# Kernel tuning notes

Hardware: AMD Instinct MI355X
Metric: run time of the kernel (lower is better)

The kernel has to match this reference:

```python
import jax, jax.numpy as jnp
import numpy as np

N = 20000   # nodes
E = 320000  # edges
T = 12      # sequence_length
H = 64      # hidden_dim
CIN = 16    # input_dim_per_step
L = 3       # num_st_layers
BN_EPS = 1e-5


def setup_inputs() -> dict:
    key = jax.random.key(0)
    ks = jax.random.split(key, 30)
    s = 0.05
    rn = lambda k, shp: jax.random.normal(k, shp, jnp.float32) * s
    inp = {
        "x": jax.random.normal(ks[0], (N, T * CIN), jnp.float32),
        "edge_index": jax.random.randint(ks[1], (2, E), 0, N, jnp.int32),
        # embedding
        "We": rn(ks[2], (CIN, H)), "be": rn(ks[3], (H,)),
        # stacked per-layer params for the 3 ST layers
        "gcn_W": rn(ks[4], (L, H, H)), "gcn_b": rn(ks[5], (L, H)),
        "conv_w": rn(ks[6], (L, H, H, 3)), "conv_b": rn(ks[7], (L, H)),
        "bn_g": jnp.ones((L, H), jnp.float32), "bn_b": rn(ks[8], (L, H)),
        "bn_m": rn(ks[9], (L, H)),
        "bn_v": jax.random.uniform(ks[10], (L, H), jnp.float32, 0.5, 1.5),
        # temporal attention MLP (H -> H//2 -> 1)
        "ta_w1": rn(ks[11], (H, H // 2)), "ta_b1": rn(ks[12], (H // 2,)),
        "ta_w2": rn(ks[13], (H // 2, 1)), "ta_b2": rn(ks[14], (1,)),
        # feature attention MLP (T -> T//2 -> 1)
        "fa_w1": rn(ks[15], (T, T // 2)), "fa_b1": rn(ks[16], (T // 2,)),
        "fa_w2": rn(ks[17], (T // 2, 1)), "fa_b2": rn(ks[18], (1,)),
        # output MLP (H -> H//2 -> 1)
        "ow1": rn(ks[19], (H, H // 2)), "ob1": rn(ks[20], (H // 2,)),
        "ow2": rn(ks[21], (H // 2, 1)), "ob2": rn(ks[22], (1,)),
    }
    return inp


def reference(x, edge_index, We, be, gcn_W, gcn_b, conv_w, conv_b,
              bn_g, bn_b, bn_m, bn_v, ta_w1, ta_b1, ta_w2, ta_b2,
              fa_w1, fa_b1, fa_w2, fa_b2, ow1, ob1, ow2, ob2):
    n = x.shape[0]
    # --- GCN normalization with self-loops (PyG gcn_norm) ---
    loops = jnp.arange(n, dtype=edge_index.dtype)
    src = jnp.concatenate([edge_index[0], loops])
    dst = jnp.concatenate([edge_index[1], loops])
    deg = jax.ops.segment_sum(jnp.ones_like(src, jnp.float32), dst, num_segments=n)
    dinv = 1.0 / jnp.sqrt(deg)  # deg >= 1 thanks to self-loops
    coef = dinv[src] * dinv[dst]  # [E+N]

    # --- per-timestep embedding (vectorized over t) ---
    xr = x.reshape(n, T, CIN)
    emb = jax.nn.relu(jnp.einsum('ntc,ch->nth', xr, We) + be)  # [N,T,H]
    x_st = emb.reshape(n, T * H)

    # --- ST layers (replicating original row-major .view layout mixing) ---
    for i in range(L):
        xi = x_st.reshape(n, H, T)  # [N,C,T]
        # GCNConv per timestep, batched over t: linear then normalized aggregate
        h = jnp.einsum('nct,cd->ndt', xi, gcn_W[i])          # [N,H,T]
        msg = coef[:, None, None] * h[src]                   # [E+N,H,T]
        agg = jax.ops.segment_sum(msg, dst, num_segments=n) + gcn_b[i][None, :, None]
        # temporal conv (kernel 3, pad 1) over T
        tmp = jax.lax.conv_general_dilated(
            agg, conv_w[i], (1,), [(1, 1)],
            dimension_numbers=('NCH', 'OIH', 'NCH')) + conv_b[i][None, :, None]
        # BatchNorm1d (eval mode: running stats)
        normed = (tmp - bn_m[i][None, :, None]) / jnp.sqrt(bn_v[i][None, :, None] + BN_EPS)
        normed = normed * bn_g[i][None, :, None] + bn_b[i][None, :, None]
        # residual is Identity (in_channels == out_channels)
        x_st = jax.nn.relu(normed + xi).reshape(n, H * T)

    # --- dual attention pooling ---
    xa = x_st.reshape(n, T, H)
    tw = (jnp.einsum('ntm,mk->ntk', jax.nn.relu(jnp.einsum('nth,hm->ntm', xa, ta_w1) + ta_b1), ta_w2) + ta_b2)[..., 0]
    tw = jax.nn.softmax(tw, axis=1)                          # [N,T]
    xt = (xa * tw[..., None]).transpose(0, 2, 1)             # [N,H,T]
    fw = (jnp.einsum('nhm,mk->nhk', jax.nn.relu(jnp.einsum('nht,tm->nhm', xt, fa_w1) + fa_b1), fa_w2) + fa_b2)[..., 0]
    fw = jax.nn.softmax(fw, axis=1)                          # [N,H]
    x_final = jnp.sum(xt * fw[..., None], axis=2)            # [N,H]

    # --- output MLP (dropout is identity in eval) ---
    out = jax.nn.relu(x_final @ ow1 + ob1) @ ow2 + ob2       # [N,1]
    return out
```

## Files before the change

kernel.cpp:

```cpp
#include <hip/hip_runtime.h>
#include <cstddef>
#include <cstdint>

#define T_ 12
#define H_ 64
#define CIN_ 16
#define F_ 768
#define PAD_ROW 772
#define BN_EPS 1e-5f
#define ECAP 80
#define RPITCH 88

typedef float v2f __attribute__((ext_vector_type(2)));
typedef short s8v __attribute__((ext_vector_type(8)));
typedef float f4v __attribute__((ext_vector_type(4)));

__device__ __forceinline__ unsigned short f2bf(float f) {
    unsigned u = __float_as_uint(f);
    unsigned r = (u + 0x7FFFu + ((u >> 16) & 1u)) >> 16;
    return (unsigned short)r;
}
__device__ __forceinline__ float bf2f(unsigned short h) {
    return __uint_as_float(((unsigned)h) << 16);
}
__device__ __forceinline__ v2f bf2x2(unsigned u) {
    v2f r;
    r.x = __uint_as_float(u << 16);
    r.y = __uint_as_float(u & 0xFFFF0000u);
    return r;
}
__device__ __forceinline__ v2f pkfma(v2f a, v2f b, v2f c) {
    return __builtin_elementwise_fma(a, b, c);
}


__global__ void k_init(int* __restrict__ cnt, int* __restrict__ cursor, int n) {
    int i = blockIdx.x * 256 + threadIdx.x;
    if (i < n) { cnt[i] = 0; cursor[i] = 0; }
}

__global__ void k_count(const int* __restrict__ dstv, int* __restrict__ cnt, int e) {
    int i = blockIdx.x * 256 + threadIdx.x;
    if (i < e) atomicAdd(&cnt[dstv[i]], 1);
}

__global__ __launch_bounds__(1024) void k_scan1(const int* __restrict__ cnt,
                                                int* __restrict__ row_local,
                                                int* __restrict__ bsum, int n) {
    __shared__ int sd[1024];
    int tid = threadIdx.x;
    int i = blockIdx.x * 1024 + tid;
    int v = (i < n) ? cnt[i] : 0;
    sd[tid] = v;
    __syncthreads();
    for (int off = 1; off < 1024; off <<= 1) {
        int t = (tid >= off) ? sd[tid - off] : 0;
        __syncthreads();
        sd[tid] += t;
        __syncthreads();
    }
    if (i < n) row_local[i] = sd[tid] - v;
    if (tid == 1023) bsum[blockIdx.x] = sd[1023];
}

__global__ __launch_bounds__(64) void k_scan2(const int* __restrict__ bsum,
                                              int* __restrict__ boff, int nb,
                                              int* __restrict__ row_start, int n) {
    int lane = threadIdx.x;
    int orig = (lane < nb) ? bsum[lane] : 0;
    int v = orig;
    for (int off = 1; off < 64; off <<= 1) {
        int t = __shfl_up(v, off);
        if (lane >= off) v += t;
    }
    if (lane < nb) boff[lane] = v - orig;
    if (lane == 63) row_start[n] = v;
}

__global__ __launch_bounds__(1024) void k_scan3(const int* __restrict__ row_local,
                                                const int* __restrict__ boff,
                                                const int* __restrict__ cnt,
                                                int* __restrict__ row_start,
                                                float* __restrict__ dinv, int n) {
    int i = blockIdx.x * 1024 + threadIdx.x;
    if (i < n) {
        row_start[i] = row_local[i] + boff[blockIdx.x];
        dinv[i] = rsqrtf((float)(cnt[i] + 1));
    }
}

__global__ void k_scatter(const int* __restrict__ srcv, const int* __restrict__ dstv,
                          const int* __restrict__ row_start, int* __restrict__ cursor,
                          const float* __restrict__ dinv, int* __restrict__ csr_src,
                          float* __restrict__ csr_coef, int e) {
    int i = blockIdx.x * 256 + threadIdx.x;
    if (i < e) {
        int d = dstv[i], s = srcv[i];
        int pos = atomicAdd(&cursor[d], 1);
        int idx = row_start[d] + pos;
        csr_src[idx]  = s;
        csr_coef[idx] = dinv[s] * dinv[d];
    }
}


__global__ __launch_bounds__(256) void k_wprep(const float* __restrict__ gcn_W,
                                               const float* __restrict__ gcn_b,
                                               const float* __restrict__ conv_w,
                                               float* __restrict__ wkp,
                                               float* __restrict__ bkp) {
    int b = blockIdx.x;
    int l = b / 12, k = (b / 4) % 3, cq = b & 3;
    const float* Wg = gcn_W + (size_t)l * 4096;
    const float* cw = conv_w + (size_t)l * 12288;
    int tid = threadIdx.x;
#pragma unroll
    for (int j = 0; j < 4; j++) {
        int idx = j * 256 + tid;
        int c = cq * 16 + (idx >> 6);
        int o = idx & 63;
        float acc = 0.f;
        for (int d = 0; d < 64; d++)
            acc += Wg[c * 64 + d] * cw[(size_t)(o * 64 + d) * 3 + k];
        wkp[(((size_t)l * 3 + k) * 64 + c) * 64 + o] = acc;
    }
    if (cq == 0 && tid < 64) {
        int o = tid;
        const float* gb = gcn_b + (size_t)l * 64;
        float acc = 0.f;
        for (int d = 0; d < 64; d++)
            acc += gb[d] * cw[(size_t)(o * 64 + d) * 3 + k];
        bkp[((size_t)l * 3 + k) * 64 + o] = acc;
    }
}

__global__ __launch_bounds__(64) void k_wpack(const float* __restrict__ wkp,
                                              unsigned short* __restrict__ wkA) {
    int b = blockIdx.x;
    int l = b / 24, rem = b % 24;
    int mt = rem / 6, ks = rem % 6;
    int lane = threadIdx.x;
    int o = mt * 16 + (lane & 15);
    int kbase = ks * 32 + (lane >> 4) * 8;
#pragma unroll
    for (int j = 0; j < 8; j++) {
        int k = kbase + j;
        int kk = k >> 6, c = k & 63;
        float v = wkp[(((size_t)l * 3 + kk) * 64 + c) * 64 + o];
        wkA[((((size_t)l * 24) + mt * 6 + ks) * 64 + lane) * 8 + j] = f2bf(v);
    }
}


__global__ __launch_bounds__(256) void k_embed(const float* __restrict__ x,
                                               const float* __restrict__ We,
                                               const float* __restrict__ be,
                                               unsigned short* __restrict__ xbf,
                                               int nT) {
    __shared__ float sW[CIN_ * H_];
    __shared__ float sb[H_];
    for (int i = threadIdx.x; i < CIN_ * H_; i += 256) sW[i] = We[i];
    if (threadIdx.x < H_) sb[threadIdx.x] = be[threadIdx.x];
    __syncthreads();
    int h4  = threadIdx.x & 15;
    int ntl = threadIdx.x >> 4;
    int nt  = blockIdx.x * 16 + ntl;
    if (nt >= nT) return;
    const float4* xp = (const float4*)(x + (size_t)nt * CIN_);
    float4 xv4[4];
    xv4[0] = xp[0]; xv4[1] = xp[1]; xv4[2] = xp[2]; xv4[3] = xp[3];
    const float* xs = (const float*)xv4;
    float acc[4];
#pragma unroll
    for (int j = 0; j < 4; j++) acc[j] = sb[h4 * 4 + j];
#pragma unroll
    for (int c = 0; c < CIN_; c++) {
        float4 w = *(const float4*)&sW[c * H_ + h4 * 4];
        float xc = xs[c];
        acc[0] += xc * w.x; acc[1] += xc * w.y; acc[2] += xc * w.z; acc[3] += xc * w.w;
    }
    ushort4 h;
    h.x = f2bf(fmaxf(acc[0], 0.f)); h.y = f2bf(fmaxf(acc[1], 0.f));
    h.z = f2bf(fmaxf(acc[2], 0.f)); h.w = f2bf(fmaxf(acc[3], 0.f));
    *(ushort4*)&xbf[(size_t)nt * H_ + h4 * 4] = h;
}


#define BPK(aL, aH, c2, u) { \
    aL = pkfma(bf2x2((u).x), c2, aL); \
    aH = pkfma(bf2x2((u).y), c2, aH); }

__global__ __launch_bounds__(256, 6) void k_layer(
        const unsigned short* __restrict__ xin,
        unsigned short* __restrict__ xout,
        const int* __restrict__ row_start, const int* __restrict__ csr_src,
        const float* __restrict__ csr_coef, const float* __restrict__ dinv,
        const unsigned short* __restrict__ wkA,
        const float* __restrict__ bkp,
        const float* __restrict__ cb,
        const float* __restrict__ bng, const float* __restrict__ bnb,
        const float* __restrict__ bnm, const float* __restrict__ bnv,
        int n) {
    __shared__ unsigned short sxb[8 * 14 * RPITCH];
    __shared__ int se[4 * ECAP * 2];
    int tid = threadIdx.x;
    int n0 = blockIdx.x * 8;
    int wave = tid >> 6, lane = tid & 63;
    int wbase = wave * (ECAP * 2);

    for (int i = tid; i < 8 * 2 * RPITCH; i += 256) {
        int s = i / (2 * RPITCH);
        int r = i - s * (2 * RPITCH);
        int row = (r < RPITCH) ? 0 : 13;
        int c = (r < RPITCH) ? r : r - RPITCH;
        sxb[s * 14 * RPITCH + row * RPITCH + c] = 0;
    }

    int begs[2], cnts[2], stgs[2], epos[2];
    {
        int pos = 0;
#pragma unroll
        for (int si = 0; si < 2; si++) {
            int nn = n0 + wave * 2 + si; if (nn >= n) nn = n - 1;
            int beg = row_start[nn], end = row_start[nn + 1];
            int cnt = end - beg;
            int stg = min(cnt, ECAP - pos);
            for (int i = lane; i < stg; i += 64) {
                se[wbase + (pos + i) * 2]     = csr_src[beg + i];
                se[wbase + (pos + i) * 2 + 1] = __float_as_int(csr_coef[beg + i]);
            }
            begs[si] = beg; cnts[si] = cnt; stgs[si] = stg; epos[si] = pos;
            pos += stg;
        }
    }

    {
        int i0 = 3 * lane;
#pragma unroll
        for (int si = 0; si < 2; si++) {
            int s = wave * 2 + si;
            int nn = n0 + s; if (nn >= n) nn = n - 1;
            float dn = dinv[nn];
            float cs = dn * dn;
            v2f cs2 = {cs, cs};
            const uint2* xp = (const uint2*)(xin + (size_t)nn * F_);
            uint2 u0 = xp[i0], u1 = xp[i0 + 1], u2 = xp[i0 + 2];
            v2f a0 = bf2x2(u0.x) * cs2, a1 = bf2x2(u0.y) * cs2;
            v2f a2 = bf2x2(u1.x) * cs2, a3 = bf2x2(u1.y) * cs2;
            v2f a4 = bf2x2(u2.x) * cs2, a5 = bf2x2(u2.y) * cs2;
            int cnt = stgs[si];
            int base = wbase + epos[si] * 2;
            int e = 0;
            for (; e + 3 < cnt; e += 4) {
                int2 p0 = *(const int2*)&se[base + e * 2];
                int2 p1 = *(const int2*)&se[base + e * 2 + 2];
                int2 p2 = *(const int2*)&se[base + e * 2 + 4];
                int2 p3 = *(const int2*)&se[base + e * 2 + 6];
                const uint2* pA = (const uint2*)(xin + (size_t)p0.x * F_);
                const uint2* pB = (const uint2*)(xin + (size_t)p1.x * F_);
                const uint2* pC = (const uint2*)(xin + (size_t)p2.x * F_);
                const uint2* pD = (const uint2*)(xin + (size_t)p3.x * F_);
                uint2 uA0 = pA[i0], uA1 = pA[i0 + 1], uA2 = pA[i0 + 2];
                uint2 uB0 = pB[i0], uB1 = pB[i0 + 1], uB2 = pB[i0 + 2];
                uint2 uC0 = pC[i0], uC1 = pC[i0 + 1], uC2 = pC[i0 + 2];
                uint2 uD0 = pD[i0], uD1 = pD[i0 + 1], uD2 = pD[i0 + 2];
                float cA = __int_as_float(p0.y), cB = __int_as_float(p1.y);
                float cC = __int_as_float(p2.y), cD = __int_as_float(p3.y);
                v2f cA2 = {cA, cA}, cB2 = {cB, cB}, cC2 = {cC, cC}, cD2 = {cD, cD};
                BPK(a0, a1, cA2, uA0) BPK(a2, a3, cA2, uA1) BPK(a4, a5, cA2, uA2)
                BPK(a0, a1, cB2, uB0) BPK(a2, a3, cB2, uB1) BPK(a4, a5, cB2, uB2)
                BPK(a0, a1, cC2, uC0) BPK(a2, a3, cC2, uC1) BPK(a4, a5, cC2, uC2)
                BPK(a0, a1, cD2, uD0) BPK(a2, a3, cD2, uD1) BPK(a4, a5, cD2, uD2)
            }
            for (; e < cnt; e++) {
                int2 p0 = *(const int2*)&se[base + e * 2];
                const uint2* pA = (const uint2*)(xin + (size_t)p0.x * F_);
                uint2 uA0 = pA[i0], uA1 = pA[i0 + 1], uA2 = pA[i0 + 2];
                float cA = __int_as_float(p0.y);
                v2f cA2 = {cA, cA};
                BPK(a0, a1, cA2, uA0) BPK(a2, a3, cA2, uA1) BPK(a4, a5, cA2, uA2)
            }
            for (int g = begs[si] + stgs[si]; g < begs[si] + cnts[si]; g++) {
                int srcI = csr_src[g];
                float cf = csr_coef[g];
                const uint2* pA = (const uint2*)(xin + (size_t)srcI * F_);
                uint2 uA0 = pA[i0], uA1 = pA[i0 + 1], uA2 = pA[i0 + 2];
                v2f cf2 = {cf, cf};
                BPK(a0, a1, cf2, uA0) BPK(a2, a3, cf2, uA1) BPK(a4, a5, cf2, uA2)
            }
            unsigned short* wp = &sxb[s * 14 * RPITCH + RPITCH + lane];
            float vals[12] = {a0.x, a0.y, a1.x, a1.y, a2.x, a2.y,
                              a3.x, a3.y, a4.x, a4.y, a5.x, a5.y};
#pragma unroll
            for (int t = 0; t < 12; t++) wp[t * RPITCH] = f2bf(vals[t]);
        }
    }
    __syncthreads();

    {
        int mt = wave;
        int q = lane >> 4;
        int l15 = lane & 15;
        s8v afr[6];
        const s8v* Ap = (const s8v*)wkA;
#pragma unroll
        for (int ks = 0; ks < 6; ks++) afr[ks] = Ap[(mt * 6 + ks) * 64 + lane];
        int obase = mt * 16 + q * 4;
        float scl[4], shf[4], ball[4], bk0a[4], bk2a[4];
#pragma unroll
        for (int r = 0; r < 4; r++) {
            int o = obase + r;
            float sc = bng[o] * rsqrtf(bnv[o] + BN_EPS);
            scl[r] = sc;
            shf[r] = bnb[o] - bnm[o] * sc;
            float b0 = bkp[o], b1 = bkp[64 + o], b2 = bkp[128 + o];
            ball[r] = cb[o] + b0 + b1 + b2;
            bk0a[r] = b0; bk2a[r] = b2;
        }
#pragma unroll
        for (int nt = 0; nt < 6; nt++) {
            int nidx = nt * 16 + l15;
            int s = nidx / 12, t = nidx - 12 * s;
            const s8v* bp = (const s8v*)&sxb[s * 14 * RPITCH + t * RPITCH + q * 8];
            f4v acc = {0.f, 0.f, 0.f, 0.f};
            acc = __builtin_amdgcn_mfma_f32_16x16x32_bf16(afr[0], bp[0],  acc, 0, 0, 0);
            acc = __builtin_amdgcn_mfma_f32_16x16x32_bf16(afr[1], bp[4],  acc, 0, 0, 0);
            acc = __builtin_amdgcn_mfma_f32_16x16x32_bf16(afr[2], bp[11], acc, 0, 0, 0);
            acc = __builtin_amdgcn_mfma_f32_16x16x32_bf16(afr[3], bp[15], acc, 0, 0, 0);
            acc = __builtin_amdgcn_mfma_f32_16x16x32_bf16(afr[4], bp[22], acc, 0, 0, 0);
            acc = __builtin_amdgcn_mfma_f32_16x16x32_bf16(afr[5], bp[26], acc, 0, 0, 0);
            int nnode = n0 + s;
            bool valid = (nnode < n);
            int rn = valid ? nnode : (n - 1);
            const unsigned short* rrow = xin + (size_t)rn * F_;
            unsigned short* orow = xout + (size_t)rn * F_;
#pragma unroll
            for (int r = 0; r < 4; r++) {
                int o = obase + r;
                float bias = ball[r];
                if (t == 0)  bias -= bk0a[r];
                if (t == 11) bias -= bk2a[r];
                float v = (acc[r] + bias) * scl[r] + shf[r] + bf2f(rrow[o * 12 + t]);
                v = fmaxf(v, 0.f);
                if (valid) orow[o * 12 + t] = f2bf(v);
            }
        }
    }
}


__global__ __launch_bounds__(128) void k_attn(const unsigned short* __restrict__ xst,
        const float* __restrict__ taw1, const float* __restrict__ tab1,
        const float* __restrict__ taw2, const float* __restrict__ tab2,
        const float* __restrict__ faw1, const float* __restrict__ fab1,
        const float* __restrict__ faw2, const float* __restrict__ fab2,
        const float* __restrict__ ow1, const float* __restrict__ ob1,
        const float* __restrict__ ow2, const float* __restrict__ ob2,
        float* __restrict__ out, int n) {
    __shared__ float sT[8 * PAD_ROW];
    __shared__ float s_tab1[32], s_taw2[32], s_ob1[32], s_ow2[32];
    __shared__ float s_faw1[72], s_fab1[8], s_faw2[8];
    __shared__ float s_tw[8 * 12];
    __shared__ float s_xf[8 * 65];
    int tid = threadIdx.x;
    int n0 = blockIdx.x * 8;
    if (tid < 32) {
        s_tab1[tid] = tab1[tid]; s_taw2[tid] = taw2[tid];
        s_ob1[tid] = ob1[tid];   s_ow2[tid] = ow2[tid];
    }
    if (tid < 72) s_faw1[tid] = faw1[tid];
    if (tid < 6) { s_fab1[tid] = fab1[tid]; s_faw2[tid] = faw2[tid]; }
    float tb2 = tab2[0], fb2 = fab2[0], o_b2 = ob2[0];
    for (int i = tid; i < 8 * F_; i += 128) {
        int s = i / F_, j = i - s * F_;
        int t = j >> 6, hh = j & 63;
        int nn = n0 + s; if (nn >= n) nn = n - 1;
        sT[s * PAD_ROW + hh * 12 + t] = bf2f(xst[(size_t)nn * F_ + j]);
    }
    __syncthreads();

    int s = tid >> 4, m2 = tid & 15;
    {
        v2f a[12];
        v2f bb = *((const v2f*)s_tab1 + m2);
#pragma unroll
        for (int t = 0; t < 12; t++) a[t] = bb;
        const float* xr = &sT[s * PAD_ROW];
        const v2f* twp = (const v2f*)taw1 + m2;
        for (int hh = 0; hh < 64; hh++) {
            float4 q0 = *(const float4*)&xr[hh * 12];
            float4 q1 = *(const float4*)&xr[hh * 12 + 4];
            float4 q2 = *(const float4*)&xr[hh * 12 + 8];
            float xv[12] = {q0.x, q0.y, q0.z, q0.w, q1.x, q1.y, q1.z, q1.w, q2.x, q2.y, q2.z, q2.w};
            v2f wv = twp[hh * 16];
#pragma unroll
            for (int t = 0; t < 12; t++)
                a[t] = pkfma(wv, (v2f){xv[t], xv[t]}, a[t]);
        }
        float w20 = s_taw2[2 * m2], w21 = s_taw2[2 * m2 + 1];
#pragma unroll
        for (int t = 0; t < 12; t++) {
            float p = fmaxf(a[t].x, 0.f) * w20 + fmaxf(a[t].y, 0.f) * w21;
            p += __shfl_xor(p, 1); p += __shfl_xor(p, 2);
            p += __shfl_xor(p, 4); p += __shfl_xor(p, 8);
            if (m2 == 0) s_tw[s * 12 + t] = p + tb2;
        }
    }
    __syncthreads();

    int wave = tid >> 6, lane = tid & 63;
    for (int q = 0; q < 4; q++) {
        int ss = wave * 4 + q;
        float tw[12];
#pragma unroll
        for (int t = 0; t < 12; t++) tw[t] = s_tw[ss * 12 + t];
        float mx = tw[0];
#pragma unroll
        for (int t = 1; t < 12; t++) mx = fmaxf(mx, tw[t]);
        float sum = 0.f;
#pragma unroll
        for (int t = 0; t < 12; t++) { tw[t] = __expf(tw[t] - mx); sum += tw[t]; }
        float inv = 1.f / sum;
        const float* xr = &sT[ss * PAD_ROW + lane * 12];
        float4 q0 = *(const float4*)(xr);
        float4 q1 = *(const float4*)(xr + 4);
        float4 q2 = *(const float4*)(xr + 8);
        float xv[12] = {q0.x, q0.y, q0.z, q0.w, q1.x, q1.y, q1.z, q1.w, q2.x, q2.y, q2.z, q2.w};
        float xt[12];
#pragma unroll
        for (int t = 0; t < 12; t++) xt[t] = xv[t] * tw[t] * inv;
        float lf = fb2;
#pragma unroll
        for (int mm = 0; mm < 6; mm++) {
            float v = s_fab1[mm];
#pragma unroll
            for (int t = 0; t < 12; t++) v += xt[t] * s_faw1[t * 6 + mm];
            lf += fmaxf(v, 0.f) * s_faw2[mm];
        }
        float m2v = lf;
#pragma unroll
        for (int off = 32; off >= 1; off >>= 1) m2v = fmaxf(m2v, __shfl_xor(m2v, off));
        float e = __expf(lf - m2v);
        float se = e;
#pragma unroll
        for (int off = 32; off >= 1; off >>= 1) se += __shfl_xor(se, off);
        float fwv = e / se;
        float xs = 0.f;
#pragma unroll
        for (int t = 0; t < 12; t++) xs += xt[t];
        s_xf[ss * 65 + lane] = fwv * xs;
    }
    __syncthreads();

    {
        float v0 = s_ob1[2 * m2], v1 = s_ob1[2 * m2 + 1];
        const float* xfp = &s_xf[s * 65];
        for (int hh = 0; hh < 64; hh++) {
            float xv = xfp[hh];
            float2 wv = *(const float2*)&ow1[hh * 32 + 2 * m2];
            v0 += xv * wv.x;
            v1 += xv * wv.y;
        }
        float p = fmaxf(v0, 0.f) * s_ow2[2 * m2] + fmaxf(v1, 0.f) * s_ow2[2 * m2 + 1];
        p += __shfl_xor(p, 1); p += __shfl_xor(p, 2);
        p += __shfl_xor(p, 4); p += __shfl_xor(p, 8);
        if (m2 == 0 && n0 + s < n) out[n0 + s] = p + o_b2;
    }
}


extern "C" void kernel_launch(void* const* d_in, const int* in_sizes, int n_in,
                              void* d_out, int out_size, void* d_ws, size_t ws_size,
                              hipStream_t stream) {
    const float* x      = (const float*)d_in[0];
    const int*   ei     = (const int*)d_in[1];
    const float* We     = (const float*)d_in[2];
    const float* be     = (const float*)d_in[3];
    const float* gcn_W  = (const float*)d_in[4];
    const float* gcn_b  = (const float*)d_in[5];
    const float* conv_w = (const float*)d_in[6];
    const float* conv_b = (const float*)d_in[7];
    const float* bn_g   = (const float*)d_in[8];
    const float* bn_b   = (const float*)d_in[9];
    const float* bn_m   = (const float*)d_in[10];
    const float* bn_v   = (const float*)d_in[11];
    const float* ta_w1  = (const float*)d_in[12];
    const float* ta_b1  = (const float*)d_in[13];
    const float* ta_w2  = (const float*)d_in[14];
    const float* ta_b2  = (const float*)d_in[15];
    const float* fa_w1  = (const float*)d_in[16];
    const float* fa_b1  = (const float*)d_in[17];
    const float* fa_w2  = (const float*)d_in[18];
    const float* fa_b2  = (const float*)d_in[19];
    const float* ow1    = (const float*)d_in[20];
    const float* ob1    = (const float*)d_in[21];
    const float* ow2    = (const float*)d_in[22];
    const float* ob2    = (const float*)d_in[23];

    int n = in_sizes[0] / (T_ * CIN_);
    int e = in_sizes[1] / 2;
    const int* srcv = ei;
    const int* dstv = ei + e;

    char* p = (char*)d_ws;
    auto take = [&](size_t bytes) -> void* {
        void* r = (void*)p;
        p += (bytes + 255) & ~(size_t)255;
        return r;
    };
    int*   cnt       = (int*)take((size_t)n * 4);
    int*   cursor    = (int*)take((size_t)n * 4);
    int*   row_start = (int*)take(((size_t)n + 1) * 4);
    int*   row_local = (int*)take((size_t)n * 4);
    int*   bsum      = (int*)take(1024 * 4);
    int*   boff      = (int*)take(1024 * 4);
    float* dinv      = (float*)take((size_t)n * 4);
    int*   csr_src   = (int*)take((size_t)e * 4);
    float* csr_coef  = (float*)take((size_t)e * 4);
    float* wkp       = (float*)take((size_t)3 * 3 * 64 * 64 * 4);
    float* bkp       = (float*)take((size_t)3 * 3 * 64 * 4);
    unsigned short* wkA = (unsigned short*)take((size_t)3 * 24 * 64 * 8 * 2);
    unsigned short* xabf = (unsigned short*)take((size_t)n * F_ * 2);
    unsigned short* xbbf = (unsigned short*)take((size_t)n * F_ * 2);

    int nb_n = (n + 255) / 256;
    int nb_e = (e + 255) / 256;
    int nb_s = (n + 1023) / 1024;

    k_wprep<<<36, 256, 0, stream>>>(gcn_W, gcn_b, conv_w, wkp, bkp);
    k_wpack<<<72, 64, 0, stream>>>(wkp, wkA);
    k_init<<<nb_n, 256, 0, stream>>>(cnt, cursor, n);
    k_count<<<nb_e, 256, 0, stream>>>(dstv, cnt, e);
    k_scan1<<<nb_s, 1024, 0, stream>>>(cnt, row_local, bsum, n);
    k_scan2<<<1, 64, 0, stream>>>(bsum, boff, nb_s, row_start, n);
    k_scan3<<<nb_s, 1024, 0, stream>>>(row_local, boff, cnt, row_start, dinv, n);
    k_scatter<<<nb_e, 256, 0, stream>>>(srcv, dstv, row_start, cursor, dinv,
                                        csr_src, csr_coef, e);

    int nT = n * T_;
    k_embed<<<(nT + 15) / 16, 256, 0, stream>>>(x, We, be, xabf, nT);

    int nb8 = (n + 7) / 8;
    const unsigned short* curbf = xabf;
    for (int i = 0; i < 3; i++) {
        unsigned short* nxtbf = (curbf == xabf) ? xbbf : xabf;
        k_layer<<<nb8, 256, 0, stream>>>(curbf, nxtbf,
                                         row_start, csr_src, csr_coef, dinv,
                                         wkA + (size_t)i * 24 * 64 * 8,
                                         bkp + (size_t)i * 3 * 64,
                                         conv_b + (size_t)i * H_,
                                         bn_g + (size_t)i * H_, bn_b + (size_t)i * H_,
                                         bn_m + (size_t)i * H_, bn_v + (size_t)i * H_,
                                         n);
        curbf = nxtbf;
    }

    k_attn<<<nb8, 128, 0, stream>>>(curbf, ta_w1, ta_b1, ta_w2, ta_b2,
                                    fa_w1, fa_b1, fa_w2, fa_b2,
                                    ow1, ob1, ow2, ob2, (float*)d_out, n);
}
```

Measured before the change: 487.0 us.

## Degree-sort nodes for balanced layer blocks and vectorize residual epilogue

Adds a counting sort of nodes by in-degree and a permutation that puts heavy and light nodes together in each 8-node block (waves take ranks w and 7-w), so that per-block gather work in the layer kernel is more even. The layer epilogue now stages the BN output in shared memory and applies the residual add and ReLU with 16-byte coalesced loads and stores, replacing scattered 2-byte global accesses. The attention load also reads four bf16 values per access. In exchange there are four extra small setup kernels, and the permuted block order loses the locality that came from consecutive node ids.

```diff
diff --git a/kernel.cpp b/kernel.cpp
--- a/kernel.cpp
+++ b/kernel.cpp
@@ -10,6 +10,7 @@
 #define BN_EPS 1e-5f
 #define ECAP 80
 #define RPITCH 88
+#define DBINS 1024
 
 typedef float v2f __attribute__((ext_vector_type(2)));
 typedef short s8v __attribute__((ext_vector_type(8)));
@@ -34,9 +35,11 @@
 }
 
 
-__global__ void k_init(int* __restrict__ cnt, int* __restrict__ cursor, int n) {
+__global__ void k_init(int* __restrict__ cnt, int* __restrict__ cursor,
+                       int* __restrict__ hist, int* __restrict__ hcur, int n) {
     int i = blockIdx.x * 256 + threadIdx.x;
     if (i < n) { cnt[i] = 0; cursor[i] = 0; }
+    if (i < DBINS) { hist[i] = 0; hcur[i] = 0; }
 }
 
 __global__ void k_count(const int* __restrict__ dstv, int* __restrict__ cnt, int e) {
@@ -104,6 +107,53 @@
 }
 
 
+__global__ void k_hist(const int* __restrict__ cnt, int* __restrict__ hist, int n) {
+    int i = blockIdx.x * 256 + threadIdx.x;
+    if (i < n) {
+        int d = min(cnt[i], DBINS - 1);
+        atomicAdd(&hist[d], 1);
+    }
+}
+
+__global__ __launch_bounds__(1024) void k_hscan(const int* __restrict__ hist,
+                                                int* __restrict__ hoff, int n) {
+    __shared__ int sd[DBINS];
+    int tid = threadIdx.x;
+    int v = hist[tid];
+    sd[tid] = v;
+    __syncthreads();
+    for (int off = 1; off < DBINS; off <<= 1) {
+        int t = (tid >= off) ? sd[tid - off] : 0;
+        __syncthreads();
+        sd[tid] += t;
+        __syncthreads();
+    }
+    hoff[tid] = n - sd[tid];
+}
+
+__global__ void k_place(const int* __restrict__ cnt, const int* __restrict__ hoff,
+                        int* __restrict__ hcur, int* __restrict__ sorted, int n) {
+    int i = blockIdx.x * 256 + threadIdx.x;
+    if (i < n) {
+        int d = min(cnt[i], DBINS - 1);
+        int pos = atomicAdd(&hcur[d], 1);
+        sorted[hoff[d] + pos] = i;
+    }
+}
+
+__global__ void k_perm(const int* __restrict__ sorted, int* __restrict__ perm,
+                       int nb, int n) {
+    int i = blockIdx.x * 256 + threadIdx.x;
+    if (i < nb * 8) {
+        int b = i >> 3, s = i & 7;
+        int w = s >> 1, si = s & 1;
+        int j = si ? (7 - w) : w;
+        int rank = j * nb + b;
+        perm[i] = (rank < n) ? sorted[rank] : -1;
+    }
+}
+
+
 __global__ __launch_bounds__(256) void k_wprep(const float* __restrict__ gcn_W,
                                                const float* __restrict__ gcn_b,
                                                const float* __restrict__ conv_w,
@@ -195,13 +245,14 @@
         unsigned short* __restrict__ xout,
         const int* __restrict__ row_start, const int* __restrict__ csr_src,
         const float* __restrict__ csr_coef, const float* __restrict__ dinv,
+        const int* __restrict__ perm,
         const unsigned short* __restrict__ wkA,
         const float* __restrict__ bkp,
         const float* __restrict__ cb,
         const float* __restrict__ bng, const float* __restrict__ bnb,
         const float* __restrict__ bnm, const float* __restrict__ bnv,
         int n) {
-    __shared__ unsigned short sxb[8 * 14 * RPITCH];
+    __shared__ __align__(16) unsigned short sxb[8 * 14 * RPITCH];
     __shared__ int se[4 * ECAP * 2];
     int tid = threadIdx.x;
     int n0 = blockIdx.x * 8;
@@ -216,14 +267,16 @@
         sxb[s * 14 * RPITCH + row * RPITCH + c] = 0;
     }
 
-    int begs[2], cnts[2], stgs[2], epos[2];
+    int begs[2], cnts[2], stgs[2], epos[2], nodes[2];
     {
         int pos = 0;
 #pragma unroll
         for (int si = 0; si < 2; si++) {
-            int nn = n0 + wave * 2 + si; if (nn >= n) nn = n - 1;
+            int pmv = perm[n0 + wave * 2 + si];
+            int nn = (pmv >= 0) ? pmv : 0;
+            nodes[si] = pmv;
             int beg = row_start[nn], end = row_start[nn + 1];
-            int cnt = end - beg;
+            int cnt = (pmv >= 0) ? (end - beg) : 0;
             int stg = min(cnt, ECAP - pos);
             for (int i = lane; i < stg; i += 64) {
                 se[wbase + (pos + i) * 2]     = csr_src[beg + i];
@@ -239,7 +292,7 @@
 #pragma unroll
         for (int si = 0; si < 2; si++) {
             int s = wave * 2 + si;
-            int nn = n0 + s; if (nn >= n) nn = n - 1;
+            int nn = (nodes[si] >= 0) ? nodes[si] : 0;
             float dn = dinv[nn];
             float cs = dn * dn;
             v2f cs2 = {cs, cs};
@@ -297,54 +350,80 @@
     }
     __syncthreads();
 
-    {
-        int mt = wave;
-        int q = lane >> 4;
-        int l15 = lane & 15;
-        s8v afr[6];
-        const s8v* Ap = (const s8v*)wkA;
-#pragma unroll
-        for (int ks = 0; ks < 6; ks++) afr[ks] = Ap[(mt * 6 + ks) * 64 + lane];
-        int obase = mt * 16 + q * 4;
-        float scl[4], shf[4], ball[4], bk0a[4], bk2a[4];
+    int mt = wave;
+    int q = lane >> 4;
+    int l15 = lane & 15;
+    s8v afr[6];
+    const s8v* Ap = (const s8v*)wkA;
+#pragma unroll
+    for (int ks = 0; ks < 6; ks++) afr[ks] = Ap[(mt * 6 + ks) * 64 + lane];
+    int obase = mt * 16 + q * 4;
+    float scl[4], shf[4], ball[4], bk0a[4], bk2a[4];
+#pragma unroll
+    for (int r = 0; r < 4; r++) {
+        int o = obase + r;
+        float sc = bng[o] * rsqrtf(bnv[o] + BN_EPS);
+        scl[r] = sc;
+        shf[r] = bnb[o] - bnm[o] * sc;
+        float b0 = bkp[o], b1 = bkp[64 + o], b2 = bkp[128 + o];
+        ball[r] = cb[o] + b0 + b1 + b2;
+        bk0a[r] = b0; bk2a[r] = b2;
+    }
+    f4v accv[6];
+#pragma unroll
+    for (int nt = 0; nt < 6; nt++) {
+        int nidx = nt * 16 + l15;
+        int s = nidx / 12, t = nidx - 12 * s;
+        const s8v* bp = (const s8v*)&sxb[s * 14 * RPITCH + t * RPITCH + q * 8];
+        f4v acc = {0.f, 0.f, 0.f, 0.f};
+        acc = __builtin_amdgcn_mfma_f32_16x16x32_bf16(afr[0], bp[0],  acc, 0, 0, 0);
+        acc = __builtin_amdgcn_mfma_f32_16x16x32_bf16(afr[1], bp[4],  acc, 0, 0, 0);
+        acc = __builtin_amdgcn_mfma_f32_16x16x32_bf16(afr[2], bp[11], acc, 0, 0, 0);
+        acc = __builtin_amdgcn_mfma_f32_16x16x32_bf16(afr[3], bp[15], acc, 0, 0, 0);
+        acc = __builtin_amdgcn_mfma_f32_16x16x32_bf16(afr[4], bp[22], acc, 0, 0, 0);
+        acc = __builtin_amdgcn_mfma_f32_16x16x32_bf16(afr[5], bp[26], acc, 0, 0, 0);
+        accv[nt] = acc;
+    }
+    __syncthreads();
+
+#pragma unroll
+    for (int nt = 0; nt < 6; nt++) {
+        int nidx = nt * 16 + l15;
+        int s = nidx / 12, t = nidx - 12 * s;
+        unsigned short* dp = &sxb[s * F_ + t];
 #pragma unroll
         for (int r = 0; r < 4; r++) {
-            int o = obase + r;
-            float sc = bng[o] * rsqrtf(bnv[o] + BN_EPS);
-            scl[r] = sc;
-            shf[r] = bnb[o] - bnm[o] * sc;
-            float b0 = bkp[o], b1 = bkp[64 + o], b2 = bkp[128 + o];
-            ball[r] = cb[o] + b0 + b1 + b2;
-            bk0a[r] = b0; bk2a[r] = b2;
-        }
-#pragma unroll
-        for (int nt = 0; nt < 6; nt++) {
-            int nidx = nt * 16 + l15;
-            int s = nidx / 12, t = nidx - 12 * s;
-            const s8v* bp = (const s8v*)&sxb[s * 14 * RPITCH + t * RPITCH + q * 8];
-            f4v acc = {0.f, 0.f, 0.f, 0.f};
-            acc = __builtin_amdgcn_mfma_f32_16x16x32_bf16(afr[0], bp[0],  acc, 0, 0, 0);
-            acc = __builtin_amdgcn_mfma_f32_16x16x32_bf16(afr[1], bp[4],  acc, 0, 0, 0);
-            acc = __builtin_amdgcn_mfma_f32_16x16x32_bf16(afr[2], bp[11], acc, 0, 0, 0);
-            acc = __builtin_amdgcn_mfma_f32_16x16x32_bf16(afr[3], bp[15], acc, 0, 0, 0);
-            acc = __builtin_amdgcn_mfma_f32_16x16x32_bf16(afr[4], bp[22], acc, 0, 0, 0);
-            acc = __builtin_amdgcn_mfma_f32_16x16x32_bf16(afr[5], bp[26], acc, 0, 0, 0);
-            int nnode = n0 + s;
-            bool valid = (nnode < n);
-            int rn = valid ? nnode : (n - 1);
-            const unsigned short* rrow = xin + (size_t)rn * F_;
-            unsigned short* orow = xout + (size_t)rn * F_;
-#pragma unroll
-            for (int r = 0; r < 4; r++) {
-                int o = obase + r;
-                float bias = ball[r];
-                if (t == 0)  bias -= bk0a[r];
-                if (t == 11) bias -= bk2a[r];
-                float v = (acc[r] + bias) * scl[r] + shf[r] + bf2f(rrow[o * 12 + t]);
-                v = fmaxf(v, 0.f);
-                if (valid) orow[o * 12 + t] = f2bf(v);
-            }
-        }
+            float bias = ball[r];
+            if (t == 0)  bias -= bk0a[r];
+            if (t == 11) bias -= bk2a[r];
+            float v = (accv[nt][r] + bias) * scl[r] + shf[r];
+            dp[(obase + r) * 12] = f2bf(v);
+        }
+    }
+    __syncthreads();
+
+#pragma unroll
+    for (int cidx = 0; cidx < 3; cidx++) {
+        int c = cidx * 256 + tid;
+        int s = c / 96, off = c - s * 96;
+        int pmv = perm[n0 + s];
+        if (pmv < 0) continue;
+        uint4 dv = *(const uint4*)&sxb[s * F_ + off * 8];
+        const uint4* rrow = (const uint4*)(xin + (size_t)pmv * F_);
+        uint4 rv = rrow[off];
+        uint4 ov;
+        unsigned* dvp = (unsigned*)&dv;
+        unsigned* rvp = (unsigned*)&rv;
+        unsigned* ovp = (unsigned*)&ov;
+#pragma unroll
+        for (int w = 0; w < 4; w++) {
+            v2f d2 = bf2x2(dvp[w]);
+            v2f r2 = bf2x2(rvp[w]);
+            float lo = fmaxf(d2.x + r2.x, 0.f);
+            float hi = fmaxf(d2.y + r2.y, 0.f);
+            ovp[w] = (unsigned)f2bf(lo) | ((unsigned)f2bf(hi) << 16);
+        }
+        *(uint4*)(xout + (size_t)pmv * F_ + off * 8) = ov;
     }
 }
 
@@ -371,11 +450,16 @@
     if (tid < 72) s_faw1[tid] = faw1[tid];
     if (tid < 6) { s_fab1[tid] = fab1[tid]; s_faw2[tid] = faw2[tid]; }
     float tb2 = tab2[0], fb2 = fab2[0], o_b2 = ob2[0];
-    for (int i = tid; i < 8 * F_; i += 128) {
+    for (int i = tid * 4; i < 8 * F_; i += 512) {
         int s = i / F_, j = i - s * F_;
+        int nn = n0 + s; if (nn >= n) nn = n - 1;
+        ushort4 v = *(const ushort4*)&xst[(size_t)nn * F_ + j];
         int t = j >> 6, hh = j & 63;
-        int nn = n0 + s; if (nn >= n) nn = n - 1;
-        sT[s * PAD_ROW + hh * 12 + t] = bf2f(xst[(size_t)nn * F_ + j]);
+        float* dst = &sT[s * PAD_ROW + hh * 12 + t];
+        dst[0]  = bf2f(v.x);
+        dst[12] = bf2f(v.y);
+        dst[24] = bf2f(v.z);
+        dst[36] = bf2f(v.w);
     }
     __syncthreads();
 
@@ -517,6 +601,11 @@
     float* dinv      = (float*)take((size_t)n * 4);
     int*   csr_src   = (int*)take((size_t)e * 4);
     float* csr_coef  = (float*)take((size_t)e * 4);
+    int*   hist      = (int*)take(DBINS * 4);
+    int*   hcur      = (int*)take(DBINS * 4);
+    int*   hoff      = (int*)take(DBINS * 4);
+    int*   sorted    = (int*)take((size_t)n * 4);
+    int*   perm      = (int*)take(((size_t)n + 8) * 4);
     float* wkp       = (float*)take((size_t)3 * 3 * 64 * 64 * 4);
     float* bkp       = (float*)take((size_t)3 * 3 * 64 * 4);
     unsigned short* wkA = (unsigned short*)take((size_t)3 * 24 * 64 * 8 * 2);
@@ -526,26 +615,30 @@
     int nb_n = (n + 255) / 256;
     int nb_e = (e + 255) / 256;
     int nb_s = (n + 1023) / 1024;
+    int nb8  = (n + 7) / 8;
 
     k_wprep<<<36, 256, 0, stream>>>(gcn_W, gcn_b, conv_w, wkp, bkp);
     k_wpack<<<72, 64, 0, stream>>>(wkp, wkA);
-    k_init<<<nb_n, 256, 0, stream>>>(cnt, cursor, n);
+    k_init<<<nb_n, 256, 0, stream>>>(cnt, cursor, hist, hcur, n);
     k_count<<<nb_e, 256, 0, stream>>>(dstv, cnt, e);
     k_scan1<<<nb_s, 1024, 0, stream>>>(cnt, row_local, bsum, n);
     k_scan2<<<1, 64, 0, stream>>>(bsum, boff, nb_s, row_start, n);
     k_scan3<<<nb_s, 1024, 0, stream>>>(row_local, boff, cnt, row_start, dinv, n);
     k_scatter<<<nb_e, 256, 0, stream>>>(srcv, dstv, row_start, cursor, dinv,
                                         csr_src, csr_coef, e);
+    k_hist<<<nb_n, 256, 0, stream>>>(cnt, hist, n);
+    k_hscan<<<1, 1024, 0, stream>>>(hist, hoff, n);
+    k_place<<<nb_n, 256, 0, stream>>>(cnt, hoff, hcur, sorted, n);
+    k_perm<<<(nb8 * 8 + 255) / 256, 256, 0, stream>>>(sorted, perm, nb8, n);
 
     int nT = n * T_;
     k_embed<<<(nT + 15) / 16, 256, 0, stream>>>(x, We, be, xabf, nT);
 
-    int nb8 = (n + 7) / 8;
     const unsigned short* curbf = xabf;
     for (int i = 0; i < 3; i++) {
         unsigned short* nxtbf = (curbf == xabf) ? xbbf : xabf;
         k_layer<<<nb8, 256, 0, stream>>>(curbf, nxtbf,
-                                         row_start, csr_src, csr_coef, dinv,
+                                         row_start, csr_src, csr_coef, dinv, perm,
                                          wkA + (size_t)i * 24 * 64 * 8,
                                          bkp + (size_t)i * 3 * 64,
                                          conv_b + (size_t)i * H_,
```

Measured after the change: 596.5 us. 22.5% more time.

## Stage layer epilogue through shared memory for coalesced residual reads and output writes

Applied to the files above, without the earlier changes.

The layer kernel now keeps the MFMA accumulators in registers, syncs, and writes the BN-scaled results into the shared buffer in node-row layout. A second pass then reads the residual and writes the output as 16-byte vectors per thread, replacing scattered 2-byte global reads and writes. The attention kernel's staging loop also switches to 4-element vector loads, and the occupancy hint is raised from 6 to 7 blocks per CU. The cost is two extra block barriers and higher register pressure from holding six accumulators, which the larger occupancy hint could make worse through spilling.

```diff
diff --git a/kernel.cpp b/kernel.cpp
--- a/kernel.cpp
+++ b/kernel.cpp
@@ -190,7 +190,7 @@
     aL = pkfma(bf2x2((u).x), c2, aL); \
     aH = pkfma(bf2x2((u).y), c2, aH); }
 
-__global__ __launch_bounds__(256, 6) void k_layer(
+__global__ __launch_bounds__(256, 7) void k_layer(
         const unsigned short* __restrict__ xin,
         unsigned short* __restrict__ xout,
         const int* __restrict__ row_start, const int* __restrict__ csr_src,
@@ -201,7 +201,7 @@
         const float* __restrict__ bng, const float* __restrict__ bnb,
         const float* __restrict__ bnm, const float* __restrict__ bnv,
         int n) {
-    __shared__ unsigned short sxb[8 * 14 * RPITCH];
+    __shared__ __align__(16) unsigned short sxb[8 * 14 * RPITCH];
     __shared__ int se[4 * ECAP * 2];
     int tid = threadIdx.x;
     int n0 = blockIdx.x * 8;
@@ -297,54 +297,80 @@
     }
     __syncthreads();
 
-    {
-        int mt = wave;
-        int q = lane >> 4;
-        int l15 = lane & 15;
-        s8v afr[6];
-        const s8v* Ap = (const s8v*)wkA;
-#pragma unroll
-        for (int ks = 0; ks < 6; ks++) afr[ks] = Ap[(mt * 6 + ks) * 64 + lane];
-        int obase = mt * 16 + q * 4;
-        float scl[4], shf[4], ball[4], bk0a[4], bk2a[4];
+    int mt = wave;
+    int q = lane >> 4;
+    int l15 = lane & 15;
+    s8v afr[6];
+    const s8v* Ap = (const s8v*)wkA;
+#pragma unroll
+    for (int ks = 0; ks < 6; ks++) afr[ks] = Ap[(mt * 6 + ks) * 64 + lane];
+    int obase = mt * 16 + q * 4;
+    float scl[4], shf[4], ball[4], bk0a[4], bk2a[4];
+#pragma unroll
+    for (int r = 0; r < 4; r++) {
+        int o = obase + r;
+        float sc = bng[o] * rsqrtf(bnv[o] + BN_EPS);
+        scl[r] = sc;
+        shf[r] = bnb[o] - bnm[o] * sc;
+        float b0 = bkp[o], b1 = bkp[64 + o], b2 = bkp[128 + o];
+        ball[r] = cb[o] + b0 + b1 + b2;
+        bk0a[r] = b0; bk2a[r] = b2;
+    }
+    f4v accv[6];
+#pragma unroll
+    for (int nt = 0; nt < 6; nt++) {
+        int nidx = nt * 16 + l15;
+        int s = nidx / 12, t = nidx - 12 * s;
+        const s8v* bp = (const s8v*)&sxb[s * 14 * RPITCH + t * RPITCH + q * 8];
+        f4v acc = {0.f, 0.f, 0.f, 0.f};
+        acc = __builtin_amdgcn_mfma_f32_16x16x32_bf16(afr[0], bp[0],  acc, 0, 0, 0);
+        acc = __builtin_amdgcn_mfma_f32_16x16x32_bf16(afr[1], bp[4],  acc, 0, 0, 0);
+        acc = __builtin_amdgcn_mfma_f32_16x16x32_bf16(afr[2], bp[11], acc, 0, 0, 0);
+        acc = __builtin_amdgcn_mfma_f32_16x16x32_bf16(afr[3], bp[15], acc, 0, 0, 0);
+        acc = __builtin_amdgcn_mfma_f32_16x16x32_bf16(afr[4], bp[22], acc, 0, 0, 0);
+        acc = __builtin_amdgcn_mfma_f32_16x16x32_bf16(afr[5], bp[26], acc, 0, 0, 0);
+        accv[nt] = acc;
+    }
+    __syncthreads();
+
+#pragma unroll
+    for (int nt = 0; nt < 6; nt++) {
+        int nidx = nt * 16 + l15;
+        int s = nidx / 12, t = nidx - 12 * s;
+        unsigned short* dp = &sxb[s * F_ + t];
 #pragma unroll
         for (int r = 0; r < 4; r++) {
-            int o = obase + r;
-            float sc = bng[o] * rsqrtf(bnv[o] + BN_EPS);
-            scl[r] = sc;
-            shf[r] = bnb[o] - bnm[o] * sc;
-            float b0 = bkp[o], b1 = bkp[64 + o], b2 = bkp[128 + o];
-            ball[r] = cb[o] + b0 + b1 + b2;
-            bk0a[r] = b0; bk2a[r] = b2;
-        }
-#pragma unroll
-        for (int nt = 0; nt < 6; nt++) {
-            int nidx = nt * 16 + l15;
-            int s = nidx / 12, t = nidx - 12 * s;
-            const s8v* bp = (const s8v*)&sxb[s * 14 * RPITCH + t * RPITCH + q * 8];
-            f4v acc = {0.f, 0.f, 0.f, 0.f};
-            acc = __builtin_amdgcn_mfma_f32_16x16x32_bf16(afr[0], bp[0],  acc, 0, 0, 0);
-            acc = __builtin_amdgcn_mfma_f32_16x16x32_bf16(afr[1], bp[4],  acc, 0, 0, 0);
-            acc = __builtin_amdgcn_mfma_f32_16x16x32_bf16(afr[2], bp[11], acc, 0, 0, 0);
-            acc = __builtin_amdgcn_mfma_f32_16x16x32_bf16(afr[3], bp[15], acc, 0, 0, 0);
-            acc = __builtin_amdgcn_mfma_f32_16x16x32_bf16(afr[4], bp[22], acc, 0, 0, 0);
-            acc = __builtin_amdgcn_mfma_f32_16x16x32_bf16(afr[5], bp[26], acc, 0, 0, 0);
-            int nnode = n0 + s;
-            bool valid = (nnode < n);
-            int rn = valid ? nnode : (n - 1);
-            const unsigned short* rrow = xin + (size_t)rn * F_;
-            unsigned short* orow = xout + (size_t)rn * F_;
-#pragma unroll
-            for (int r = 0; r < 4; r++) {
-                int o = obase + r;
-                float bias = ball[r];
-                if (t == 0)  bias -= bk0a[r];
-                if (t == 11) bias -= bk2a[r];
-                float v = (acc[r] + bias) * scl[r] + shf[r] + bf2f(rrow[o * 12 + t]);
-                v = fmaxf(v, 0.f);
-                if (valid) orow[o * 12 + t] = f2bf(v);
-            }
-        }
+            float bias = ball[r];
+            if (t == 0)  bias -= bk0a[r];
+            if (t == 11) bias -= bk2a[r];
+            float v = (accv[nt][r] + bias) * scl[r] + shf[r];
+            dp[(obase + r) * 12] = f2bf(v);
+        }
+    }
+    __syncthreads();
+
+#pragma unroll
+    for (int cidx = 0; cidx < 3; cidx++) {
+        int c = cidx * 256 + tid;
+        int s = c / 96, off = c - s * 96;
+        int nn = n0 + s;
+        if (nn >= n) continue;
+        uint4 dv = *(const uint4*)&sxb[s * F_ + off * 8];
+        const uint4* rrow = (const uint4*)(xin + (size_t)nn * F_);
+        uint4 rv = rrow[off];
+        uint4 ov;
+        unsigned* dvp = (unsigned*)&dv;
+        unsigned* rvp = (unsigned*)&rv;
+        unsigned* ovp = (unsigned*)&ov;
+#pragma unroll
+        for (int w = 0; w < 4; w++) {
+            v2f d2 = bf2x2(dvp[w]);
+            v2f r2 = bf2x2(rvp[w]);
+            float lo = fmaxf(d2.x + r2.x, 0.f);
+            float hi = fmaxf(d2.y + r2.y, 0.f);
+            ovp[w] = (unsigned)f2bf(lo) | ((unsigned)f2bf(hi) << 16);
+        }
+        *(uint4*)(xout + (size_t)nn * F_ + off * 8) = ov;
     }
 }
 
@@ -371,11 +397,16 @@
     if (tid < 72) s_faw1[tid] = faw1[tid];
     if (tid < 6) { s_fab1[tid] = fab1[tid]; s_faw2[tid] = faw2[tid]; }
     float tb2 = tab2[0], fb2 = fab2[0], o_b2 = ob2[0];
-    for (int i = tid; i < 8 * F_; i += 128) {
+    for (int i = tid * 4; i < 8 * F_; i += 512) {
         int s = i / F_, j = i - s * F_;
+        int nn = n0 + s; if (nn >= n) nn = n - 1;
+        ushort4 v = *(const ushort4*)&xst[(size_t)nn * F_ + j];
         int t = j >> 6, hh = j & 63;
-        int nn = n0 + s; if (nn >= n) nn = n - 1;
-        sT[s * PAD_ROW + hh * 12 + t] = bf2f(xst[(size_t)nn * F_ + j]);
+        float* dst = &sT[s * PAD_ROW + hh * 12 + t];
+        dst[0]  = bf2f(v.x);
+        dst[12] = bf2f(v.y);
+        dst[24] = bf2f(v.z);
+        dst[36] = bf2f(v.w);
     }
     __syncthreads();
 
@@ -526,6 +557,7 @@
     int nb_n = (n + 255) / 256;
     int nb_e = (e + 255) / 256;
     int nb_s = (n + 1023) / 1024;
+    int nb8  = (n + 7) / 8;
 
     k_wprep<<<36, 256, 0, stream>>>(gcn_W, gcn_b, conv_w, wkp, bkp);
     k_wpack<<<72, 64, 0, stream>>>(wkp, wkA);
@@ -540,7 +572,6 @@
     int nT = n * T_;
     k_embed<<<(nT + 15) / 16, 256, 0, stream>>>(x, We, be, xabf, nT);
 
-    int nb8 = (n + 7) / 8;
     const unsigned short* curbf = xabf;
     for (int i = 0; i < 3; i++) {
         unsigned short* nxtbf = (curbf == xabf) ? xbbf : xabf;
```

Result: no change. 482.4 us (-0.9%).
